# Optimization experiments

Measured on AMD Instinct MI355X. Metric: run time of the kernel, lower is better.

Reference implementation:

```python
import jax, jax.numpy as jnp
import numpy as np

MAX_LAG_FRACTION = 0.25


def setup_inputs() -> dict:
    key = jax.random.key(0)
    k1, k2, k3 = jax.random.split(key, 3)
    B, T, D = 64, 1024, 2
    alpha_pred = jax.random.uniform(k1, (B,), dtype=jnp.float32) * 2.0  # alpha in (0, 2)
    trajectory = jax.random.normal(k2, (B, T, D), dtype=jnp.float32)
    lengths = jax.random.randint(k3, (B,), T // 2, T + 1, dtype=jnp.int64)
    return {"alpha_pred": alpha_pred, "trajectory": trajectory, "lengths": lengths}


def reference(alpha_pred, trajectory, lengths):
    B, T, D = trajectory.shape
    max_lag = max(1, int(T * MAX_LAG_FRACTION))  # static; lags beyond length are masked
    lags_i = jnp.arange(1, max_lag + 1)                      # (L,)
    log_lags = jnp.log(lags_i.astype(jnp.float32))           # (L,)
    P = T - 1
    positions = jnp.arange(P)                                # (P,)

    end_idx = positions[None, :] + lags_i[:, None]           # (L, P)
    pos_valid = end_idx < T                                  # (L, P)
    end_c = jnp.minimum(end_idx, T - 1)

    traj_end = trajectory[:, end_c, :]                       # (B, L, P, D) gather
    traj_start = trajectory[:, :P, :][:, None, :, :]         # (B, 1, P, D)
    disp = traj_end - traj_start                             # (B, L, P, D)

    # valid if position < length - lag (and end index in-bounds)
    sample_valid = positions[None, None, :] < (lengths[:, None, None] - lags_i[None, :, None])
    valid = (pos_valid[None, :, :] & sample_valid).astype(jnp.float32)  # (B, L, P)

    sq_disp = jnp.sum(disp * disp, axis=-1)                  # (B, L, P)
    counts = jnp.maximum(jnp.sum(valid, axis=-1), 1.0)       # (B, L)
    msd = jnp.sum(sq_disp * valid, axis=-1) / counts         # (B, L)

    lag_mask = (lengths[:, None] > lags_i[None, :]).astype(jnp.float32)  # (B, L)
    log_msd = jnp.log(msd + 1e-8)                            # (B, L)

    alpha = alpha_pred[:, None]                              # (B, 1)
    resid = log_msd - alpha * log_lags[None, :]
    denom = jnp.maximum(jnp.sum(lag_mask, axis=1), 1.0)      # (B,)
    intercept = jnp.sum(resid * lag_mask, axis=1) / denom    # (B,)

    sq_err = (alpha * log_lags[None, :] + intercept[:, None] - log_msd) ** 2
    per_traj = jnp.sum(sq_err * lag_mask, axis=1) / denom
    return jnp.mean(per_traj)
```

## Files before the change

kernel.cpp:

```cpp
#include <hip/hip_runtime.h>

#define TT 1024
#define MAXLAG 256
#define NCHUNK 4
#define NQ 4
#define NWAY 16

__global__ __launch_bounds__(1024) void msd_fused(const float* __restrict__ alpha_pred,
                                                  const float* __restrict__ traj,
                                                  const int* __restrict__ lengths,
                                                  float* __restrict__ ws,
                                                  float* __restrict__ out,
                                                  int B) {
    __shared__ float s[TT * 2];
    __shared__ float sums[NQ][MAXLAG];
    __shared__ float sr[4], sm[4], se4[4];
    __shared__ unsigned sh_ref, sh_old;

    const int b = blockIdx.x >> 2;
    const int c = blockIdx.x & 3;
    const int t = threadIdx.x;

    float* partial = ws;
    float* ptraj   = ws + (size_t)B * NCHUNK * MAXLAG;
    unsigned* ctr = (unsigned*)((char*)ws + (512u << 10));

    const float4* t4 = (const float4*)(traj + (size_t)b * TT * 2);
    float4* s4 = (float4*)s;
    if (t < TT * 2 / 4) s4[t] = t4[t];

    if (t == 0)
        sh_ref = __hip_atomic_load(&ctr[65 * 16],
                                   __ATOMIC_RELAXED, __HIP_MEMORY_SCOPE_AGENT);

    const float alpha = alpha_pred[b];
    const int L = lengths[b];
    __syncthreads();
    const unsigned ref = sh_ref;

    const int wv = t >> 6;
    const int lane = t & 63;
    const int q = wv >> 2;
    const int g = (wv + q) & 3;
    const int lagIdx = g * 64 + lane;
    const int lag = lagIdx + 1;
    const int way = c * NQ + q;
    const int cnt = L - lag;

    const float2* s2 = (const float2*)s;
    float acc = 0.0f;
    int p = way;
    #pragma unroll 2
    for (; p + 16 < cnt; p += 32) {
        float2 a0 = s2[p];
        float2 a1 = s2[p + 16];
        float2 e0 = s2[p + lag];
        float2 e1 = s2[p + 16 + lag];
        float dx0 = e0.x - a0.x, dy0 = e0.y - a0.y;
        float dx1 = e1.x - a1.x, dy1 = e1.y - a1.y;
        acc += dx0 * dx0 + dy0 * dy0;
        acc += dx1 * dx1 + dy1 * dy1;
    }
    if (p < cnt) {
        float2 a = s2[p];
        float2 e = s2[p + lag];
        float dx = e.x - a.x, dy = e.y - a.y;
        acc += dx * dx + dy * dy;
    }
    sums[q][lagIdx] = acc;
    __syncthreads();

    if (t < MAXLAG) {
        float tot = sums[0][t] + sums[1][t] + sums[2][t] + sums[3][t];
        __hip_atomic_store(&partial[((size_t)b * NCHUNK + c) * MAXLAG + t], tot,
                           __ATOMIC_RELAXED, __HIP_MEMORY_SCOPE_AGENT);
    }
    __syncthreads();

    if (t == 0)
        sh_old = __hip_atomic_fetch_add(&ctr[b * 16], 1u,
                                        __ATOMIC_RELAXED, __HIP_MEMORY_SCOPE_AGENT);
    __syncthreads();
    if (sh_old - ref != NCHUNK - 1) return;

    float resid = 0.0f, mask = 0.0f, denom = 1.0f;
    if (t < MAXLAG) {
        float tot = 0.0f;
        #pragma unroll
        for (int cc = 0; cc < NCHUNK; ++cc)
            tot += __hip_atomic_load(&partial[((size_t)b * NCHUNK + cc) * MAXLAG + t],
                                     __ATOMIC_RELAXED, __HIP_MEMORY_SCOPE_AGENT);
        const float cntf = fmaxf((float)(L - lag), 1.0f);
        const float msd = tot / cntf;
        mask = (L > lag) ? 1.0f : 0.0f;
        resid = logf(msd + 1e-8f) - alpha * logf((float)lag);

        float r = resid * mask, mk = mask;
        for (int off = 32; off; off >>= 1) {
            r  += __shfl_down(r,  off, 64);
            mk += __shfl_down(mk, off, 64);
        }
        if ((t & 63) == 0) { sr[t >> 6] = r; sm[t >> 6] = mk; }
    }
    __syncthreads();

    if (t < MAXLAG) {
        const float sumr = sr[0] + sr[1] + sr[2] + sr[3];
        const float summ = sm[0] + sm[1] + sm[2] + sm[3];
        denom = fmaxf(summ, 1.0f);
        const float intercept = sumr / denom;
        const float d = intercept - resid;
        float se = d * d * mask;
        for (int off = 32; off; off >>= 1) se += __shfl_down(se, off, 64);
        if ((t & 63) == 0) se4[t >> 6] = se;
    }
    __syncthreads();

    if (t == 0) {
        const float per_traj = (se4[0] + se4[1] + se4[2] + se4[3]) / denom;
        __hip_atomic_store(&ptraj[b], per_traj,
                           __ATOMIC_RELAXED, __HIP_MEMORY_SCOPE_AGENT);
        sh_old = __hip_atomic_fetch_add(&ctr[64 * 16], 1u,
                                        __ATOMIC_RELAXED, __HIP_MEMORY_SCOPE_AGENT);
    }
    __syncthreads();
    if (sh_old - ref != (unsigned)(B - 1)) return;

    if (t < 64) {
        float v = (t < B) ? __hip_atomic_load(&ptraj[t], __ATOMIC_RELAXED,
                                              __HIP_MEMORY_SCOPE_AGENT)
                          : 0.0f;
        for (int off = 32; off; off >>= 1) v += __shfl_down(v, off, 64);
        if (t == 0) out[0] = v / (float)B;
    }
}

extern "C" void kernel_launch(void* const* d_in, const int* in_sizes, int n_in,
                              void* d_out, int out_size, void* d_ws, size_t ws_size,
                              hipStream_t stream) {
    const float* alpha = (const float*)d_in[0];
    const float* traj  = (const float*)d_in[1];
    const int*   lens  = (const int*)d_in[2];
    float* out = (float*)d_out;
    float* ws  = (float*)d_ws;

    const int B = in_sizes[0];

    msd_fused<<<dim3(B * NCHUNK), dim3(1024), 0, stream>>>(alpha, traj, lens, ws, out, B);
}
```

Measured before the change: 63.53 us.

## Drop shared-memory quarter reduction; write per-wave partials to global and unroll 4x

Each thread now stores its per-(quarter, lag) partial sum straight to the global workspace instead of combining the four quarters in shared memory behind an extra barrier. The last-arriving chunk block then sums 16 partials per lag instead of 4. The inner loop is also unrolled to four independent load pairs per iteration. This removes one __syncthreads and some LDS traffic, at the cost of four times more global partial stores and more loads in the final reduction.

```diff
diff --git a/kernel.cpp b/kernel.cpp
--- a/kernel.cpp
+++ b/kernel.cpp
@@ -13,7 +13,6 @@
                                                   float* __restrict__ out,
                                                   int B) {
     __shared__ float s[TT * 2];
-    __shared__ float sums[NQ][MAXLAG];
     __shared__ float sr[4], sm[4], se4[4];
     __shared__ unsigned sh_ref, sh_old;
 
@@ -22,8 +21,8 @@
     const int t = threadIdx.x;
 
     float* partial = ws;
-    float* ptraj   = ws + (size_t)B * NCHUNK * MAXLAG;
-    unsigned* ctr = (unsigned*)((char*)ws + (512u << 10));
+    float* ptraj   = ws + (size_t)B * NCHUNK * NQ * MAXLAG;
+    unsigned* ctr = (unsigned*)((char*)ws + (2u << 20));
 
     const float4* t4 = (const float4*)(traj + (size_t)b * TT * 2);
     float4* s4 = (float4*)s;
@@ -48,14 +47,32 @@
     const int cnt = L - lag;
 
     const float2* s2 = (const float2*)s;
+    const float2* e2 = s2 + lag;
     float acc = 0.0f;
     int p = way;
-    #pragma unroll 2
+    for (; p + 48 < cnt; p += 64) {
+        float2 a0 = s2[p];
+        float2 a1 = s2[p + 16];
+        float2 a2 = s2[p + 32];
+        float2 a3 = s2[p + 48];
+        float2 e0 = e2[p];
+        float2 e1 = e2[p + 16];
+        float2 e2v = e2[p + 32];
+        float2 e3 = e2[p + 48];
+        float dx0 = e0.x - a0.x, dy0 = e0.y - a0.y;
+        float dx1 = e1.x - a1.x, dy1 = e1.y - a1.y;
+        float dx2 = e2v.x - a2.x, dy2 = e2v.y - a2.y;
+        float dx3 = e3.x - a3.x, dy3 = e3.y - a3.y;
+        acc += dx0 * dx0 + dy0 * dy0;
+        acc += dx1 * dx1 + dy1 * dy1;
+        acc += dx2 * dx2 + dy2 * dy2;
+        acc += dx3 * dx3 + dy3 * dy3;
+    }
     for (; p + 16 < cnt; p += 32) {
         float2 a0 = s2[p];
         float2 a1 = s2[p + 16];
-        float2 e0 = s2[p + lag];
-        float2 e1 = s2[p + 16 + lag];
+        float2 e0 = e2[p];
+        float2 e1 = e2[p + 16];
         float dx0 = e0.x - a0.x, dy0 = e0.y - a0.y;
         float dx1 = e1.x - a1.x, dy1 = e1.y - a1.y;
         acc += dx0 * dx0 + dy0 * dy0;
@@ -63,18 +80,13 @@
     }
     if (p < cnt) {
         float2 a = s2[p];
-        float2 e = s2[p + lag];
+        float2 e = e2[p];
         float dx = e.x - a.x, dy = e.y - a.y;
         acc += dx * dx + dy * dy;
     }
-    sums[q][lagIdx] = acc;
-    __syncthreads();
 
-    if (t < MAXLAG) {
-        float tot = sums[0][t] + sums[1][t] + sums[2][t] + sums[3][t];
-        __hip_atomic_store(&partial[((size_t)b * NCHUNK + c) * MAXLAG + t], tot,
-                           __ATOMIC_RELAXED, __HIP_MEMORY_SCOPE_AGENT);
-    }
+    __hip_atomic_store(&partial[(((size_t)b * NCHUNK + c) * NQ + q) * MAXLAG + lagIdx],
+                       acc, __ATOMIC_RELAXED, __HIP_MEMORY_SCOPE_AGENT);
     __syncthreads();
 
     if (t == 0)
@@ -88,8 +100,11 @@
         float tot = 0.0f;
         #pragma unroll
         for (int cc = 0; cc < NCHUNK; ++cc)
-            tot += __hip_atomic_load(&partial[((size_t)b * NCHUNK + cc) * MAXLAG + t],
-                                     __ATOMIC_RELAXED, __HIP_MEMORY_SCOPE_AGENT);
+            #pragma unroll
+            for (int qq = 0; qq < NQ; ++qq)
+                tot += __hip_atomic_load(
+                    &partial[(((size_t)b * NCHUNK + cc) * NQ + qq) * MAXLAG + t],
+                    __ATOMIC_RELAXED, __HIP_MEMORY_SCOPE_AGENT);
         const float cntf = fmaxf((float)(L - lag), 1.0f);
         const float msd = tot / cntf;
         mask = (L > lag) ? 1.0f : 0.0f;
```

After: 63.50 us. No clear change (-0.1%).
